# Kernel optimization log

Measured on AMD Instinct MI355X. Metric: run time of the kernel, lower is better.

Reference implementation:

```python
import jax, jax.numpy as jnp
import numpy as np

B, S, D = 4, 2048, 2048
NH, NKV = 16, 4
HD = D // NH          # 128
GROUPS = NH // NKV    # 4
ROPE_BASE = 1000000.0


def setup_inputs() -> dict:
    key = jax.random.key(0)
    ks = jax.random.split(key, 8)
    sc = 0.02
    return {
        "x": jax.random.normal(ks[0], (B, S, D), dtype=jnp.float32),
        "wq_w": jax.random.normal(ks[1], (D, D), dtype=jnp.float32) * sc,
        "wq_b": jax.random.normal(ks[2], (D,), dtype=jnp.float32) * sc,
        "wk_w": jax.random.normal(ks[3], (NKV * HD, D), dtype=jnp.float32) * sc,
        "wk_b": jax.random.normal(ks[4], (NKV * HD,), dtype=jnp.float32) * sc,
        "wv_w": jax.random.normal(ks[5], (NKV * HD, D), dtype=jnp.float32) * sc,
        "wv_b": jax.random.normal(ks[6], (NKV * HD,), dtype=jnp.float32) * sc,
        "wo_w": jax.random.normal(ks[7], (D, D), dtype=jnp.float32) * sc,
    }


def _rope_cos_sin(seq_len, head_dim, dtype):
    inv_freq = 1.0 / (ROPE_BASE ** (jnp.arange(0, head_dim, 2, dtype=jnp.float32) / head_dim))
    t = jnp.arange(seq_len, dtype=jnp.float32)
    freqs = jnp.outer(t, inv_freq)              # [S, HD/2]
    emb = jnp.concatenate([freqs, freqs], axis=-1)  # [S, HD]
    return jnp.cos(emb).astype(dtype), jnp.sin(emb).astype(dtype)


def _rotate_half(x):
    half = x.shape[-1] // 2
    return jnp.concatenate([-x[..., half:], x[..., :half]], axis=-1)


def reference(x, wq_w, wq_b, wk_w, wk_b, wv_w, wv_b, wo_w):
    # QKV projections (wq/wk/wv have bias; out_proj does not)
    q = x @ wq_w.T + wq_b                       # [B,S,D]
    k = x @ wk_w.T + wk_b                       # [B,S,NKV*HD]
    v = x @ wv_w.T + wv_b

    q = q.reshape(B, S, NH, HD).transpose(0, 2, 1, 3)    # [B,NH,S,HD]
    k = k.reshape(B, S, NKV, HD).transpose(0, 2, 1, 3)   # [B,NKV,S,HD]
    v = v.reshape(B, S, NKV, HD).transpose(0, 2, 1, 3)

    # GQA: repeat_interleave kv heads to match q heads
    k = jnp.repeat(k, GROUPS, axis=1)                    # [B,NH,S,HD]
    v = jnp.repeat(v, GROUPS, axis=1)

    cos, sin = _rope_cos_sin(S, HD, q.dtype)             # [S,HD]
    q = q * cos + _rotate_half(q) * sin
    k = k * cos + _rotate_half(k) * sin

    scale = 1.0 / np.sqrt(HD)
    scores = jnp.einsum("bhqd,bhkd->bhqk", q, k) * scale
    causal = jnp.tril(jnp.ones((S, S), dtype=bool))
    scores = jnp.where(causal, scores, jnp.finfo(scores.dtype).min)
    probs = jax.nn.softmax(scores, axis=-1)
    ctx = jnp.einsum("bhqk,bhkd->bhqd", probs, v)        # [B,NH,S,HD]

    ctx = ctx.transpose(0, 2, 1, 3).reshape(B, S, D)     # b h s d -> b s (h d)
    return ctx @ wo_w.T                                  # [B,S,D]
```

## Files before the change

### kernel.cpp

```cpp
#include <hip/hip_runtime.h>
#include <cstdint>
#include <cstddef>

#define B_   4
#define S_   2048
#define D_   2048
#define NH_  16
#define NKV_ 4
#define HD_  128

typedef __attribute__((ext_vector_type(8))) short short8;
typedef __attribute__((ext_vector_type(4))) float f32x4;

__device__ __forceinline__ unsigned short f2bf(float f) {
    union { float f; unsigned u; } v{f};
    unsigned r = v.u + 0x7FFF + ((v.u >> 16) & 1);
    return (unsigned short)(r >> 16);
}
__device__ __forceinline__ float bf2f(unsigned short h) {
    union { unsigned u; float f; } v{(unsigned)h << 16};
    return v.f;
}
__device__ __forceinline__ void split1(float f, unsigned short& h, unsigned short& l) {
    h = f2bf(f);
    l = f2bf(f - bf2f(h));
}
__device__ __forceinline__ unsigned pack_split(float f) {
    unsigned short h, l; split1(f, h, l);
    return (unsigned)h | ((unsigned)l << 16);
}
__device__ __forceinline__ void unpack8(const unsigned* w, short8& hi, short8& lo) {
    unsigned h[4], l[4];
#pragma unroll
    for (int i = 0; i < 4; ++i) {
        h[i] = (w[2*i] & 0xFFFFu) | (w[2*i+1] << 16);
        l[i] = (w[2*i] >> 16) | (w[2*i+1] & 0xFFFF0000u);
    }
    hi = *(short8*)h; lo = *(short8*)l;
}

__global__ __launch_bounds__(256) void split_bf16_k(
    const float* __restrict__ src, ushort* __restrict__ hi, ushort* __restrict__ lo)
{
    size_t i = ((size_t)blockIdx.x * 256 + threadIdx.x) * 4;
    float4 f = *(const float4*)&src[i];
    ushort4 h, l;
    split1(f.x, h.x, l.x); split1(f.y, h.y, l.y);
    split1(f.z, h.z, l.z); split1(f.w, h.w, l.w);
    *(ushort4*)&hi[i] = h;
    *(ushort4*)&lo[i] = l;
}

__global__ __launch_bounds__(256) void gemm_mfma_split(
    const ushort* __restrict__ Ah, const ushort* __restrict__ Al,
    const ushort* __restrict__ Bh, const ushort* __restrict__ Bl,
    const float* __restrict__ bias, float* __restrict__ C,
    int M, int N, int K)
{
    __shared__ ushort sA[2][128 * 32];
    __shared__ ushort sB[2][128 * 32];

    const int tid  = threadIdx.x;
    const int wave = tid >> 6;
    const int lane = tid & 63;
    const int bm = blockIdx.y * 128;
    const int bn = blockIdx.x * 128;
    const int wm = (wave & 1) * 64;
    const int wn = (wave >> 1) * 64;

    f32x4 acc[4][4];
#pragma unroll
    for (int mt = 0; mt < 4; ++mt)
#pragma unroll
        for (int nt = 0; nt < 4; ++nt) acc[mt][nt] = 0.f;

    const ushort* gbase = (wave == 0) ? Ah : (wave == 1) ? Al : (wave == 2) ? Bh : Bl;
    ushort* sbase = (wave == 0) ? sA[0] : (wave == 1) ? sA[1] : (wave == 2) ? sB[0] : sB[1];
    const int rb   = (wave < 2) ? bm : bn;
    const int lrow = lane >> 2;
    const int lcol = (lane & 3) * 8;

    const int koff = (lane >> 4) * 8;
    const int rsel = lane & 15;

    for (int k0 = 0; k0 < K; k0 += 32) {
        __syncthreads();
        const ushort* g0 = gbase + (size_t)(rb + lrow) * K + k0 + lcol;
#pragma unroll
        for (int i = 0; i < 8; ++i) {
            __builtin_amdgcn_global_load_lds(
                (const __attribute__((address_space(1))) unsigned int*)(g0 + (size_t)i * 16 * K),
                (__attribute__((address_space(3))) unsigned int*)(sbase + i * 512),
                16, 0, 0);
        }
        __syncthreads();

        short8 a_h[4], a_l[4], b_h[4], b_l[4];
#pragma unroll
        for (int t = 0; t < 4; ++t) {
            a_h[t] = *(const short8*)&sA[0][(wm + t * 16 + rsel) * 32 + koff];
            a_l[t] = *(const short8*)&sA[1][(wm + t * 16 + rsel) * 32 + koff];
            b_h[t] = *(const short8*)&sB[0][(wn + t * 16 + rsel) * 32 + koff];
            b_l[t] = *(const short8*)&sB[1][(wn + t * 16 + rsel) * 32 + koff];
        }
#pragma unroll
        for (int mt = 0; mt < 4; ++mt)
#pragma unroll
            for (int nt = 0; nt < 4; ++nt) {
                acc[mt][nt] = __builtin_amdgcn_mfma_f32_16x16x32_bf16(a_h[mt], b_h[nt], acc[mt][nt], 0, 0, 0);
                acc[mt][nt] = __builtin_amdgcn_mfma_f32_16x16x32_bf16(a_h[mt], b_l[nt], acc[mt][nt], 0, 0, 0);
                acc[mt][nt] = __builtin_amdgcn_mfma_f32_16x16x32_bf16(a_l[mt], b_h[nt], acc[mt][nt], 0, 0, 0);
            }
    }

    const int crow0 = bm + wm + (lane >> 4) * 4;
    const int ccol0 = bn + wn + (lane & 15);
#pragma unroll
    for (int nt = 0; nt < 4; ++nt) {
        float bb = bias ? bias[ccol0 + nt * 16] : 0.f;
#pragma unroll
        for (int mt = 0; mt < 4; ++mt)
#pragma unroll
            for (int r = 0; r < 4; ++r)
                C[(size_t)(crow0 + mt * 16 + r) * N + ccol0 + nt * 16] = acc[mt][nt][r] + bb;
    }
}

__global__ __launch_bounds__(256) void rope_split_kernel(
    float* __restrict__ t, int H, float scale, int do_rope)
{
    const int tid = threadIdx.x;
    const int rid = blockIdx.x * 2 + (tid >> 7);
    const int d   = tid & 127;
    size_t fbase = (size_t)rid * 128;
    float val;
    if (do_rope) {
        const int s = (rid / H) & (S_ - 1);
        const int j = d & 63;
        float inv  = 1.0f / powf(1.0e6f, (float)j * (1.0f / 64.0f));
        float fr = (float)s * inv;
        float sn, cs; sincosf(fr, &sn, &cs);
        float x0 = t[fbase + d];
        float xp = t[fbase + (d ^ 64)];
        float rot = (d < 64) ? -xp : xp;
        val = fmaf(x0, cs, rot * sn) * scale;
    } else {
        val = t[fbase + d] * scale;
    }
    __syncthreads();
    unsigned short h, l; split1(val, h, l);
    ushort* us = (ushort*)t;
    us[(size_t)rid * 256 + d]       = h;
    us[(size_t)rid * 256 + 128 + d] = l;
}

__global__ __launch_bounds__(256, 2) void flash_attn_mfma(
    const ushort* __restrict__ Qsp, const ushort* __restrict__ Ksp,
    const ushort* __restrict__ Vsp, ushort* __restrict__ ctx_h,
    ushort* __restrict__ ctx_l)
{
    __shared__ __align__(16) ushort Ks[32][280];
    __shared__ __align__(16) unsigned Vt[128][36];
    __shared__ __align__(16) unsigned Pw[4][32][36];

    const int tid  = threadIdx.x;
    const int wave = tid >> 6;
    const int lane = tid & 63;
    const int l15  = lane & 15;
    const int quad = lane >> 4;
    const int q0   = (gridDim.x - 1 - blockIdx.x) * 128;
    const int h    = blockIdx.y;
    const int b    = blockIdx.z;
    const int kvh  = h >> 2;
    const int wq0  = q0 + wave * 32;

    short8 qf[2][4][2];
#pragma unroll
    for (int nf = 0; nf < 2; ++nf)
#pragma unroll
        for (int ks = 0; ks < 4; ++ks) {
            size_t base = (((size_t)b * S_ + wq0 + nf * 16 + l15) * NH_ + h) * 256
                        + ks * 32 + quad * 8;
            qf[nf][ks][0] = *(const short8*)&Qsp[base];
            qf[nf][ks][1] = *(const short8*)&Qsp[base + 128];
        }

    f32x4 O[2][8];
#pragma unroll
    for (int mf = 0; mf < 2; ++mf)
#pragma unroll
        for (int nf = 0; nf < 8; ++nf) O[mf][nf] = 0.f;
    float m_[2] = {-3.0e38f, -3.0e38f};
    float l_[2] = {0.f, 0.f};

    const int ntiles = q0 / 32 + 4;
    for (int t = 0; t < ntiles; ++t) {
        const int k0 = t * 32;
        __syncthreads();

#pragma unroll
        for (int i = 0; i < 4; ++i) {
            int c = tid + i * 256;
            int row = c >> 5, seg = c & 31;
            const ushort* src = Ksp + (((size_t)b * S_ + k0 + row) * NKV_ + kvh) * 256 + seg * 8;
            ushort* dst = &Ks[row][seg * 8 + (seg >= 16 ? 16 : 0)];
            *(uint4*)dst = *(const uint4*)src;
        }
        {
            int row = tid & 31, fs = tid >> 5;
            const ushort* src = Vsp + (((size_t)b * S_ + k0 + row) * NKV_ + kvh) * 256 + fs * 16;
#pragma unroll
            for (int hf = 0; hf < 2; ++hf) {
                uint4 hv = *(const uint4*)(src + hf * 8);
                uint4 lv = *(const uint4*)(src + 128 + hf * 8);
                const ushort* hp = (const ushort*)&hv;
                const ushort* lp = (const ushort*)&lv;
#pragma unroll
                for (int i = 0; i < 8; ++i)
                    Vt[fs * 16 + hf * 8 + i][row] = (unsigned)hp[i] | ((unsigned)lp[i] << 16);
            }
        }
        __syncthreads();

        f32x4 st[2][2];
#pragma unroll
        for (int nf = 0; nf < 2; ++nf)
#pragma unroll
            for (int mf = 0; mf < 2; ++mf) st[nf][mf] = 0.f;
#pragma unroll
        for (int ks = 0; ks < 4; ++ks) {
            short8 kf_h[2], kf_l[2];
#pragma unroll
            for (int mf = 0; mf < 2; ++mf) {
                kf_h[mf] = *(const short8*)&Ks[mf * 16 + l15][ks * 32 + quad * 8];
                kf_l[mf] = *(const short8*)&Ks[mf * 16 + l15][144 + ks * 32 + quad * 8];
            }
#pragma unroll
            for (int nf = 0; nf < 2; ++nf)
#pragma unroll
                for (int mf = 0; mf < 2; ++mf) {
                    st[nf][mf] = __builtin_amdgcn_mfma_f32_16x16x32_bf16(kf_h[mf], qf[nf][ks][0], st[nf][mf], 0, 0, 0);
                    st[nf][mf] = __builtin_amdgcn_mfma_f32_16x16x32_bf16(kf_h[mf], qf[nf][ks][1], st[nf][mf], 0, 0, 0);
                    st[nf][mf] = __builtin_amdgcn_mfma_f32_16x16x32_bf16(kf_l[mf], qf[nf][ks][0], st[nf][mf], 0, 0, 0);
                }
        }

        if (k0 + 31 > wq0) {
#pragma unroll
            for (int nf = 0; nf < 2; ++nf)
#pragma unroll
                for (int mf = 0; mf < 2; ++mf)
#pragma unroll
                    for (int r = 0; r < 4; ++r) {
                        int kg = k0 + mf * 16 + quad * 4 + r;
                        int qg = wq0 + nf * 16 + l15;
                        if (kg > qg) st[nf][mf][r] = -3.0e38f;
                    }
        }

        float alp[2];
#pragma unroll
        for (int nf = 0; nf < 2; ++nf) {
            float rm = -3.0e38f;
#pragma unroll
            for (int mf = 0; mf < 2; ++mf)
#pragma unroll
                for (int r = 0; r < 4; ++r) rm = fmaxf(rm, st[nf][mf][r]);
            rm = fmaxf(rm, __shfl_xor(rm, 16));
            rm = fmaxf(rm, __shfl_xor(rm, 32));
            float mn = fmaxf(m_[nf], rm);
            float a  = __expf(m_[nf] - mn);
            float rs = 0.f;
#pragma unroll
            for (int mf = 0; mf < 2; ++mf)
#pragma unroll
                for (int r = 0; r < 4; ++r) {
                    float p = __expf(st[nf][mf][r] - mn);
                    st[nf][mf][r] = p;
                    rs += p;
                }
            rs += __shfl_xor(rs, 16);
            rs += __shfl_xor(rs, 32);
            l_[nf] = l_[nf] * a + rs;
            m_[nf] = mn;
            alp[nf] = a;
        }

#pragma unroll
        for (int omf = 0; omf < 2; ++omf)
#pragma unroll
            for (int r = 0; r < 4; ++r) {
                float av = __shfl(alp[omf], (lane & 48) | (quad * 4 + r));
#pragma unroll
                for (int nf = 0; nf < 8; ++nf) O[omf][nf][r] *= av;
            }

#pragma unroll
        for (int nf = 0; nf < 2; ++nf)
#pragma unroll
            for (int mf = 0; mf < 2; ++mf) {
                uint4 w;
                w.x = pack_split(st[nf][mf][0]);
                w.y = pack_split(st[nf][mf][1]);
                w.z = pack_split(st[nf][mf][2]);
                w.w = pack_split(st[nf][mf][3]);
                *(uint4*)&Pw[wave][nf * 16 + l15][mf * 16 + quad * 4] = w;
            }
        __syncthreads();

        short8 ph[2], pl[2];
#pragma unroll
        for (int omf = 0; omf < 2; ++omf) {
            const unsigned* pw = &Pw[wave][omf * 16 + l15][quad * 8];
            unsigned w[8];
            *(uint4*)w       = *(const uint4*)pw;
            *(uint4*)(w + 4) = *(const uint4*)(pw + 4);
            unpack8(w, ph[omf], pl[omf]);
        }
#pragma unroll
        for (int vnf = 0; vnf < 8; ++vnf) {
            const unsigned* vw = &Vt[vnf * 16 + l15][quad * 8];
            unsigned w[8];
            *(uint4*)w       = *(const uint4*)vw;
            *(uint4*)(w + 4) = *(const uint4*)(vw + 4);
            short8 vh, vl;
            unpack8(w, vh, vl);
#pragma unroll
            for (int omf = 0; omf < 2; ++omf) {
                O[omf][vnf] = __builtin_amdgcn_mfma_f32_16x16x32_bf16(ph[omf], vh, O[omf][vnf], 0, 0, 0);
                O[omf][vnf] = __builtin_amdgcn_mfma_f32_16x16x32_bf16(ph[omf], vl, O[omf][vnf], 0, 0, 0);
                O[omf][vnf] = __builtin_amdgcn_mfma_f32_16x16x32_bf16(pl[omf], vh, O[omf][vnf], 0, 0, 0);
            }
        }
    }

    float li[2] = {1.f / l_[0], 1.f / l_[1]};
#pragma unroll
    for (int omf = 0; omf < 2; ++omf)
#pragma unroll
        for (int r = 0; r < 4; ++r) {
            float il = __shfl(li[omf], (lane & 48) | (quad * 4 + r));
            int qrow = wq0 + omf * 16 + quad * 4 + r;
            size_t rowb = ((size_t)b * S_ + qrow) * (size_t)D_ + h * HD_;
#pragma unroll
            for (int nf = 0; nf < 8; ++nf) {
                float val = O[omf][nf][r] * il;
                unsigned short hh, ll; split1(val, hh, ll);
                int feat = nf * 16 + l15;
                ctx_h[rowb + feat] = hh;
                ctx_l[rowb + feat] = ll;
            }
        }
}

extern "C" void kernel_launch(void* const* d_in, const int* in_sizes, int n_in,
                              void* d_out, int out_size, void* d_ws, size_t ws_size,
                              hipStream_t stream)
{
    const float* x    = (const float*)d_in[0];
    const float* wq_w = (const float*)d_in[1];
    const float* wq_b = (const float*)d_in[2];
    const float* wk_w = (const float*)d_in[3];
    const float* wk_b = (const float*)d_in[4];
    const float* wv_w = (const float*)d_in[5];
    const float* wv_b = (const float*)d_in[6];
    const float* wo_w = (const float*)d_in[7];
    float* out = (float*)d_out;

    const int M = B_ * S_;
    const size_t NX   = (size_t)M * D_;
    const size_t NKVE = (size_t)M * NKV_ * HD_;
    const size_t NWQ  = (size_t)D_ * D_;
    const size_t NWK  = (size_t)(NKV_ * HD_) * D_;

    float*  q   = (float*)d_ws;
    float*  k   = q + NX;
    float*  v   = k + NKVE;
    ushort* xh  = (ushort*)(v + NKVE);
    ushort* xl  = xh + NX;
    ushort* wqh = xl + NX;
    ushort* wql = wqh + NWQ;
    ushort* wkh = wql + NWQ;
    ushort* wkl = wkh + NWK;
    ushort* wvh = wkl + NWK;
    ushort* wvl = wvh + NWK;
    ushort* woh = wvl + NWK;
    ushort* wol = woh + NWQ;

    split_bf16_k<<<NX  / 1024, 256, 0, stream>>>(x,    xh,  xl);
    split_bf16_k<<<NWQ / 1024, 256, 0, stream>>>(wq_w, wqh, wql);
    split_bf16_k<<<NWK / 1024, 256, 0, stream>>>(wk_w, wkh, wkl);
    split_bf16_k<<<NWK / 1024, 256, 0, stream>>>(wv_w, wvh, wvl);
    split_bf16_k<<<NWQ / 1024, 256, 0, stream>>>(wo_w, woh, wol);

    gemm_mfma_split<<<dim3(D_/128,         M/128), 256, 0, stream>>>(xh, xl, wqh, wql, wq_b, q, M, D_,       D_);
    gemm_mfma_split<<<dim3((NKV_*HD_)/128, M/128), 256, 0, stream>>>(xh, xl, wkh, wkl, wk_b, k, M, NKV_*HD_, D_);
    gemm_mfma_split<<<dim3((NKV_*HD_)/128, M/128), 256, 0, stream>>>(xh, xl, wvh, wvl, wv_b, v, M, NKV_*HD_, D_);

    rope_split_kernel<<<(M * NH_)  / 2, 256, 0, stream>>>(q, NH_,  0.08838834764831845f, 1);
    rope_split_kernel<<<(M * NKV_) / 2, 256, 0, stream>>>(k, NKV_, 1.0f, 1);
    rope_split_kernel<<<(M * NKV_) / 2, 256, 0, stream>>>(v, NKV_, 1.0f, 0);

    flash_attn_mfma<<<dim3(S_/128, NH_, B_), 256, 0, stream>>>(
        (const ushort*)q, (const ushort*)k, (const ushort*)v, xh, xl);

    gemm_mfma_split<<<dim3(D_/128, M/128), 256, 0, stream>>>(xh, xl, woh, wol, nullptr, out, M, D_, D_);
}
```

Before: 1.307 ms.

## Permute K rows so P stays in registers, dropping LDS round-trip

New measurement: 1.607 ms. 1.23x slower.

```diff
diff --git a/kernel.cpp b/kernel.cpp
--- a/kernel.cpp
+++ b/kernel.cpp
@@ -154,14 +154,13 @@
     us[(size_t)rid * 256 + 128 + d] = l;
 }
 
-__global__ __launch_bounds__(256, 2) void flash_attn_mfma(
+__global__ __launch_bounds__(256, 4) void flash_attn_mfma(
     const ushort* __restrict__ Qsp, const ushort* __restrict__ Ksp,
     const ushort* __restrict__ Vsp, ushort* __restrict__ ctx_h,
     ushort* __restrict__ ctx_l)
 {
     __shared__ __align__(16) ushort Ks[32][280];
     __shared__ __align__(16) unsigned Vt[128][36];
-    __shared__ __align__(16) unsigned Pw[4][32][36];
 
     const int tid  = threadIdx.x;
     const int wave = tid >> 6;
@@ -202,8 +201,9 @@
         for (int i = 0; i < 4; ++i) {
             int c = tid + i * 256;
             int row = c >> 5, seg = c & 31;
+            int prow = ((row & 4) << 2) | ((row >> 3) << 2) | (row & 3);
             const ushort* src = Ksp + (((size_t)b * S_ + k0 + row) * NKV_ + kvh) * 256 + seg * 8;
-            ushort* dst = &Ks[row][seg * 8 + (seg >= 16 ? 16 : 0)];
+            ushort* dst = &Ks[prow][seg * 8 + (seg >= 16 ? 16 : 0)];
             *(uint4*)dst = *(const uint4*)src;
         }
         {
@@ -252,7 +252,7 @@
                 for (int mf = 0; mf < 2; ++mf)
 #pragma unroll
                     for (int r = 0; r < 4; ++r) {
-                        int kg = k0 + mf * 16 + quad * 4 + r;
+                        int kg = k0 + quad * 8 + mf * 4 + r;
                         int qg = wq0 + nf * 16 + l15;
                         if (kg > qg) st[nf][mf][r] = -3.0e38f;
                     }
@@ -295,28 +295,24 @@
                 for (int nf = 0; nf < 8; ++nf) O[omf][nf][r] *= av;
             }
 
-#pragma unroll
-        for (int nf = 0; nf < 2; ++nf)
-#pragma unroll
-            for (int mf = 0; mf < 2; ++mf) {
-                uint4 w;
-                w.x = pack_split(st[nf][mf][0]);
-                w.y = pack_split(st[nf][mf][1]);
-                w.z = pack_split(st[nf][mf][2]);
-                w.w = pack_split(st[nf][mf][3]);
-                *(uint4*)&Pw[wave][nf * 16 + l15][mf * 16 + quad * 4] = w;
-            }
-        __syncthreads();
-
         short8 ph[2], pl[2];
 #pragma unroll
         for (int omf = 0; omf < 2; ++omf) {
-            const unsigned* pw = &Pw[wave][omf * 16 + l15][quad * 8];
-            unsigned w[8];
-            *(uint4*)w       = *(const uint4*)pw;
-            *(uint4*)(w + 4) = *(const uint4*)(pw + 4);
-            unpack8(w, ph[omf], pl[omf]);
-        }
+            unsigned hu[4], lu[4];
+#pragma unroll
+            for (int mf = 0; mf < 2; ++mf)
+#pragma unroll
+                for (int pr = 0; pr < 2; ++pr) {
+                    unsigned short ah, al, bh, bl;
+                    split1(st[omf][mf][pr * 2],     ah, al);
+                    split1(st[omf][mf][pr * 2 + 1], bh, bl);
+                    hu[mf * 2 + pr] = (unsigned)ah | ((unsigned)bh << 16);
+                    lu[mf * 2 + pr] = (unsigned)al | ((unsigned)bl << 16);
+                }
+            ph[omf] = *(short8*)hu;
+            pl[omf] = *(short8*)lu;
+        }
+
 #pragma unroll
         for (int vnf = 0; vnf < 8; ++vnf) {
             const unsigned* vw = &Vt[vnf * 16 + l15][quad * 8];
```
